# Kernel tuning notes

Hardware: AMD Instinct MI355X
Metric: run time of the kernel (lower is better)

## Reference

```python
import jax, jax.numpy as jnp
import numpy as np
from jax import lax

LN_EPS = 1e-5

D_MODEL, N_HEADS, HEAD_DIM, RANK, POWER_K = 1024, 16, 64, 32, 4
RIDGE_EPS, SPECTRAL_GAMMA = 1e-4, 0.99


def setup_inputs() -> dict:
    key = jax.random.key(0)
    ks = jax.random.split(key, 8)
    B, T = 4, 4096
    s = 1.0 / np.sqrt(D_MODEL)
    inp = {
        "hidden_states": jax.random.normal(ks[0], (B, T, D_MODEL), dtype=jnp.float32),
        "Wk": jax.random.normal(ks[1], (D_MODEL, N_HEADS * RANK), dtype=jnp.float32) * s,
        "Wq": jax.random.normal(ks[2], (D_MODEL, N_HEADS * RANK), dtype=jnp.float32) * s,
        "Wv": jax.random.normal(ks[3], (D_MODEL, N_HEADS * HEAD_DIM), dtype=jnp.float32) * s,
        "Wo": jax.random.normal(ks[4], (N_HEADS * HEAD_DIM, D_MODEL), dtype=jnp.float32) * s,
        "ln_scale": jnp.ones((D_MODEL,), jnp.float32),
        "ln_bias": jnp.zeros((D_MODEL,), jnp.float32),
        "gate_alpha": jnp.zeros((1,), jnp.float32),
        "log_ridge": jnp.array(np.log(RIDGE_EPS), jnp.float32),
        "log_gamma": jnp.array(np.log(SPECTRAL_GAMMA), jnp.float32),
        "prefix_len": 2048,
    }
    return inp


def _tri_solve(L, b, transpose=False):
    # solves L x = b (or L^T x = b) with lower-triangular L; batched over leading dims
    return lax.linalg.triangular_solve(L, b, left_side=True, lower=True, transpose_a=transpose)


def _build_operator(keys, values, ridge, gamma):
    # keys: (B,H,L,r), values: (B,H,L,dh)
    r = keys.shape[-1]
    G = jnp.einsum('bhlr,bhls->bhrs', keys, keys) + ridge * jnp.eye(r, dtype=keys.dtype)
    M = jnp.einsum('bhlr,bhls->bhrs', keys[:, :, 1:, :], keys[:, :, :-1, :])
    L = jnp.linalg.cholesky(G)                       # (B,H,r,r)
    U = _tri_solve(L, M)                             # L^{-1} M
    V = _tri_solve(L, jnp.swapaxes(U, -1, -2))       # L^{-1} (L^{-1}M)^T
    A_w = jnp.swapaxes(V, -1, -2)                    # L^{-1} M L^{-T}
    gamma_c = jnp.minimum(gamma, 1.0)
    sigma = jnp.linalg.svd(A_w, compute_uv=False)[..., 0]  # spectral norm
    sigma = jnp.maximum(sigma, 1e-8)
    scale = gamma_c / jnp.maximum(sigma, 1.0)
    A_w = A_w * scale[..., None, None]
    C_v = jnp.einsum('bhld,bhlr->bhdr', values, keys)       # (B,H,dh,r)
    Y = _tri_solve(L, jnp.swapaxes(C_v, -1, -2))            # L^{-1} C_v^T
    Bv_T = _tri_solve(L, Y, transpose=True)                 # G^{-1} C_v^T
    B_v = jnp.swapaxes(Bv_T, -1, -2)                        # (B,H,dh,r)
    return A_w, L, B_v


def _spectral_filter(A_w, L, B_v, queries, power_K):
    # queries: (B,H,Q,r) -> (B,H,Q,dh)
    qT = jnp.swapaxes(queries, -1, -2)      # (B,H,r,Q)
    w = _tri_solve(L, qT)                   # whiten
    for _ in range(power_K):
        w = jnp.matmul(A_w, w)
    z_hat = jnp.matmul(L, w)                # unwhiten
    out = jnp.matmul(B_v, z_hat)            # (B,H,dh,Q)
    return jnp.swapaxes(out, -1, -2)


def reference(hidden_states, Wk, Wq, Wv, Wo, ln_scale, ln_bias,
              gate_alpha, log_ridge, log_gamma, prefix_len):
    B, T, D = hidden_states.shape
    P = max(1, min(int(prefix_len), T - 1))
    mu = jnp.mean(hidden_states, axis=-1, keepdims=True)
    var = jnp.var(hidden_states, axis=-1, keepdims=True)
    normed = (hidden_states - mu) / jnp.sqrt(var + LN_EPS) * ln_scale + ln_bias
    def proj(W, dim):
        y = normed @ W
        return jnp.swapaxes(y.reshape(B, T, N_HEADS, dim), 1, 2)  # (B,H,T,dim)
    keys_all = proj(Wk, RANK)
    queries_all = proj(Wq, RANK)
    values_all = proj(Wv, HEAD_DIM)
    ridge = jnp.exp(log_ridge)
    gamma = jnp.exp(log_gamma)
    A_w, L, B_v = _build_operator(keys_all[:, :, :P, :], values_all[:, :, :P, :], ridge, gamma)
    q_out = _spectral_filter(A_w, L, B_v, queries_all[:, :, P:, :], POWER_K)
    p_out = _spectral_filter(A_w, L, B_v, keys_all[:, :, :P, :], POWER_K)
    full = jnp.concatenate([p_out, q_out], axis=2)               # (B,H,T,dh)
    full = jnp.swapaxes(full, 1, 2).reshape(B, T, N_HEADS * HEAD_DIM)
    out = full @ Wo
    return jax.nn.sigmoid(gate_alpha) * out
```

## Files before the change

kernel.cpp:

```cpp
#include <hip/hip_runtime.h>
#include <math.h>

#define D_MODEL 1024
#define TT 4096
#define NB 4
#define NH 16
#define TCH 8

typedef __attribute__((ext_vector_type(8))) short s8v;
typedef __attribute__((ext_vector_type(4))) float f4v;
typedef __attribute__((ext_vector_type(8))) unsigned short u16x8;

#define OFF_STATS ((size_t)0)
#define OFF_GP    ((size_t)(1) << 20)
#define OFF_MP    ((size_t)(3) << 20)
#define OFF_CP    ((size_t)(5) << 20)
#define OFF_FT    ((size_t)(9) << 20)
#define OFF_WKH   ((size_t)(10) << 20)
#define OFF_WKL   ((size_t)(11) << 20)
#define OFF_WQH   ((size_t)(12) << 20)
#define OFF_WQL   ((size_t)(13) << 20)
#define OFF_WVH   ((size_t)(14) << 20)
#define OFF_WVL   ((size_t)(16) << 20)
#define OFF_WOH   ((size_t)(18) << 20)
#define OFF_WOL   ((size_t)(20) << 20)
#define OFF_Y1    ((size_t)(22) << 20)
#define OFF_Y2    ((size_t)(54) << 20)
#define OFF_FH    OFF_Y2

__device__ __forceinline__ unsigned short bf16_rne(float x) {
  unsigned u = __float_as_uint(x);
  return (unsigned short)((u + 0x7fffu + ((u >> 16) & 1u)) >> 16);
}
__device__ __forceinline__ void split_bf16(float x, unsigned short& h, unsigned short& l) {
  unsigned u = __float_as_uint(x);
  unsigned r = (u + 0x7fffu + ((u >> 16) & 1u)) & 0xffff0000u;
  h = (unsigned short)(r >> 16);
  float res = x - __uint_as_float(r);
  l = bf16_rne(res);
}

__device__ __forceinline__ void gll16(unsigned short* lds, const unsigned short* g) {
  __builtin_amdgcn_global_load_lds(
      (__attribute__((address_space(1))) void*)(void*)(g),
      (__attribute__((address_space(3))) void*)(lds), 16, 0, 0);
}

__device__ __forceinline__ void xcd_swz(int gx, int gy, int& x, int& y, int& z) {
  int wg = blockIdx.x + gx * (blockIdx.y + gy * blockIdx.z);
  int k = wg & 7, j = wg >> 3;
  x = j % gx;
  int yz = k + ((j / gx) << 3);
  y = yz % gy;
  z = yz / gy;
}

__global__ __launch_bounds__(256) void ln_stats_k(const float* __restrict__ X,
                                                  float* __restrict__ stats) {
  int r = blockIdx.x;
  const float4 v = ((const float4*)(X + (size_t)r * D_MODEL))[threadIdx.x];
  float s  = v.x + v.y + v.z + v.w;
  float ss = v.x * v.x + v.y * v.y + v.z * v.z + v.w * v.w;
#pragma unroll
  for (int off = 32; off > 0; off >>= 1) {
    s  += __shfl_down(s, off, 64);
    ss += __shfl_down(ss, off, 64);
  }
  __shared__ float as_[4], bs_[4];
  int w = threadIdx.x >> 6, lane = threadIdx.x & 63;
  if (lane == 0) { as_[w] = s; bs_[w] = ss; }
  __syncthreads();
  if (threadIdx.x == 0) {
    float S  = as_[0] + as_[1] + as_[2] + as_[3];
    float SS = bs_[0] + bs_[1] + bs_[2] + bs_[3];
    float mu  = S * (1.0f / D_MODEL);
    float var = SS * (1.0f / D_MODEL) - mu * mu;
    stats[2 * (size_t)r]     = mu;
    stats[2 * (size_t)r + 1] = 1.0f / sqrtf(var + 1e-5f);
  }
}

__global__ __launch_bounds__(256) void prep_w_k(const float* __restrict__ W, int N,
                                                unsigned short* __restrict__ Thi,
                                                unsigned short* __restrict__ Tlo) {
  __shared__ float tileT[32 * 33];
  const int n0 = blockIdx.x * 32, k0 = blockIdx.y * 32;
  const int tid = threadIdx.x;
  {
    int k_l = tid >> 3, n4 = (tid & 7) << 2;
    float4 v = *(const float4*)&W[(size_t)(k0 + k_l) * N + n0 + n4];
    tileT[(n4 + 0) * 33 + k_l] = v.x;
    tileT[(n4 + 1) * 33 + k_l] = v.y;
    tileT[(n4 + 2) * 33 + k_l] = v.z;
    tileT[(n4 + 3) * 33 + k_l] = v.w;
  }
  __syncthreads();
  {
    int n_l = tid >> 3, k4 = (tid & 7) << 2;
    unsigned short h[4], l[4];
#pragma unroll
    for (int i = 0; i < 4; i++) split_bf16(tileT[n_l * 33 + k4 + i], h[i], l[i]);
    *(ushort4*)&Thi[(size_t)(n0 + n_l) * 1024 + k0 + k4] = make_ushort4(h[0], h[1], h[2], h[3]);
    *(ushort4*)&Tlo[(size_t)(n0 + n_l) * 1024 + k0 + k4] = make_ushort4(l[0], l[1], l[2], l[3]);
  }
}

__global__ __launch_bounds__(256) void gemm_proj_k(
    const float* __restrict__ X, const float* __restrict__ stats,
    const float* __restrict__ lng, const float* __restrict__ lnb,
    const unsigned short* __restrict__ WThi, const unsigned short* __restrict__ WTlo,
    int Nw, const int* __restrict__ pref, int mode, float* __restrict__ Y) {
  int P = pref[0]; P = P < 1 ? 1 : (P > TT - 1 ? TT - 1 : P);
  int xx, yy, zz;
  xcd_swz(8, 32, xx, yy, zz);
  const int b  = zz;
  const int t0 = yy * 128;
  const int n0 = xx * 128;
  if (mode == 1) { if (t0 + 128 <= P) return; }
  else           { if (t0 >= P) return; }
  const int row0 = b * TT + t0;
  __shared__ __align__(16) unsigned short Ah[128 * 40], Al[128 * 40];
  __shared__ __align__(16) unsigned short Bh[128 * 32], Bl[128 * 32];
  __shared__ float mus[128], rss[128];
  const int tid = threadIdx.x;
  if (tid < 128) {
    mus[tid] = stats[2 * (size_t)(row0 + tid)];
    rss[tid] = stats[2 * (size_t)(row0 + tid) + 1];
  }
  const int lane = tid & 63;
  const int wid  = tid >> 6;
  const int wm = (wid >> 1) * 64, wn = (wid & 1) * 64;
  const int lm = lane & 15, lq = lane >> 4;
  const int srow = lane >> 2, scol = (lane & 3) << 3;
  f4v acc[4][4];
#pragma unroll
  for (int i = 0; i < 4; i++)
#pragma unroll
    for (int j = 0; j < 4; j++) acc[i][j] = (f4v){0.f, 0.f, 0.f, 0.f};

  for (int kt = 0; kt < D_MODEL; kt += 32) {
    __syncthreads();
#pragma unroll
    for (int s = 0; s < 2; s++) {
      int seg = wid * 2 + s;
      int brow = n0 + seg * 16 + srow;
      gll16(&Bh[seg * 512], &WThi[(size_t)brow * 1024 + kt + scol]);
      gll16(&Bl[seg * 512], &WTlo[(size_t)brow * 1024 + kt + scol]);
    }
#pragma unroll
    for (int q = 0; q < 2; q++) {
      int c = tid * 2 + q;
      int m = c >> 2, k8 = (c & 3) << 3;
      const float* src = &X[(size_t)(row0 + m) * D_MODEL + kt + k8];
      float mu = mus[m], rs = rss[m];
      u16x8 hv, lv;
#pragma unroll
      for (int i = 0; i < 8; i++) {
        float nv = (src[i] - mu) * rs * lng[kt + k8 + i] + lnb[kt + k8 + i];
        unsigned short h, l;
        split_bf16(nv, h, l);
        hv[i] = h; lv[i] = l;
      }
      *(u16x8*)&Ah[m * 40 + k8] = hv;
      *(u16x8*)&Al[m * 40 + k8] = lv;
    }
    __syncthreads();
    s8v ah[4], al[4], bh[4], bl[4];
#pragma unroll
    for (int i = 0; i < 4; i++) {
      int ar = (wm + i * 16 + lm) * 40 + lq * 8;
      int br = (wn + i * 16 + lm) * 32 + lq * 8;
      ah[i] = *(const s8v*)&Ah[ar];
      al[i] = *(const s8v*)&Al[ar];
      bh[i] = *(const s8v*)&Bh[br];
      bl[i] = *(const s8v*)&Bl[br];
    }
#pragma unroll
    for (int mi = 0; mi < 4; mi++)
#pragma unroll
      for (int ni = 0; ni < 4; ni++) {
        acc[mi][ni] = __builtin_amdgcn_mfma_f32_16x16x32_bf16(ah[mi], bh[ni], acc[mi][ni], 0, 0, 0);
        acc[mi][ni] = __builtin_amdgcn_mfma_f32_16x16x32_bf16(ah[mi], bl[ni], acc[mi][ni], 0, 0, 0);
        acc[mi][ni] = __builtin_amdgcn_mfma_f32_16x16x32_bf16(al[mi], bh[ni], acc[mi][ni], 0, 0, 0);
      }
  }
#pragma unroll
  for (int mi = 0; mi < 4; mi++) {
#pragma unroll
    for (int r = 0; r < 4; r++) {
      int t = t0 + wm + mi * 16 + lq * 4 + r;
      bool ok = (mode == 1) ? (t >= P) : (t < P);
      if (!ok) continue;
      size_t orow = (mode == 2) ? ((size_t)b * P + t) : ((size_t)b * TT + t);
#pragma unroll
      for (int ni = 0; ni < 4; ni++)
        Y[orow * Nw + n0 + wn + ni * 16 + lm] = acc[mi][ni][r];
    }
  }
}

__global__ __launch_bounds__(256) void gemm_kq_k(
    const float* __restrict__ X, const float* __restrict__ stats,
    const float* __restrict__ lng, const float* __restrict__ lnb,
    const unsigned short* __restrict__ KH, const unsigned short* __restrict__ KL,
    const unsigned short* __restrict__ QH, const unsigned short* __restrict__ QL,
    const int* __restrict__ pref, float* __restrict__ Y) {
  int P = pref[0]; P = P < 1 ? 1 : (P > TT - 1 ? TT - 1 : P);
  int xx, yy, zz;
  xcd_swz(4, 32, xx, yy, zz);
  const int b  = zz;
  const int t0 = yy * 128;
  const int n0 = xx * 128;
  const int row0 = b * TT + t0;
  const bool hasK = (t0 < P);
  const bool hasQ = (t0 + 128 > P);
  __shared__ __align__(16) unsigned short Ah[128 * 40], Al[128 * 40];
  __shared__ __align__(16) unsigned short Bh[128 * 32], Bl[128 * 32];
  __shared__ float mus[128], rss[128];
  const int tid = threadIdx.x;
  if (tid < 128) {
    mus[tid] = stats[2 * (size_t)(row0 + tid)];
    rss[tid] = stats[2 * (size_t)(row0 + tid) + 1];
  }
  const int lane = tid & 63;
  const int wid  = tid >> 6;
  const int wm = (wid >> 1) * 64, wn = (wid & 1) * 64;
  const int lm = lane & 15, lq = lane >> 4;
  const int srow = lane >> 2, scol = (lane & 3) << 3;

  for (int pass = 0; pass < 2; pass++) {
    if (pass == 0 && !hasK) continue;
    if (pass == 1 && !hasQ) continue;
    const unsigned short* WThi = pass ? QH : KH;
    const unsigned short* WTlo = pass ? QL : KL;
    f4v acc[4][4];
#pragma unroll
    for (int i = 0; i < 4; i++)
#pragma unroll
      for (int j = 0; j < 4; j++) acc[i][j] = (f4v){0.f, 0.f, 0.f, 0.f};

    for (int kt = 0; kt < D_MODEL; kt += 32) {
      __syncthreads();
#pragma unroll
      for (int s = 0; s < 2; s++) {
        int seg = wid * 2 + s;
        int brow = n0 + seg * 16 + srow;
        gll16(&Bh[seg * 512], &WThi[(size_t)brow * 1024 + kt + scol]);
        gll16(&Bl[seg * 512], &WTlo[(size_t)brow * 1024 + kt + scol]);
      }
#pragma unroll
      for (int q = 0; q < 2; q++) {
        int c = tid * 2 + q;
        int m = c >> 2, k8 = (c & 3) << 3;
        const float* src = &X[(size_t)(row0 + m) * D_MODEL + kt + k8];
        float mu = mus[m], rs = rss[m];
        u16x8 hv, lv;
#pragma unroll
        for (int i = 0; i < 8; i++) {
          float nv = (src[i] - mu) * rs * lng[kt + k8 + i] + lnb[kt + k8 + i];
          unsigned short h, l;
          split_bf16(nv, h, l);
          hv[i] = h; lv[i] = l;
        }
        *(u16x8*)&Ah[m * 40 + k8] = hv;
        *(u16x8*)&Al[m * 40 + k8] = lv;
      }
      __syncthreads();
      s8v ah[4], al[4], bh[4], bl[4];
#pragma unroll
      for (int i = 0; i < 4; i++) {
        int ar = (wm + i * 16 + lm) * 40 + lq * 8;
        int br = (wn + i * 16 + lm) * 32 + lq * 8;
        ah[i] = *(const s8v*)&Ah[ar];
        al[i] = *(const s8v*)&Al[ar];
        bh[i] = *(const s8v*)&Bh[br];
        bl[i] = *(const s8v*)&Bl[br];
      }
#pragma unroll
      for (int mi = 0; mi < 4; mi++)
#pragma unroll
        for (int ni = 0; ni < 4; ni++) {
          acc[mi][ni] = __builtin_amdgcn_mfma_f32_16x16x32_bf16(ah[mi], bh[ni], acc[mi][ni], 0, 0, 0);
          acc[mi][ni] = __builtin_amdgcn_mfma_f32_16x16x32_bf16(ah[mi], bl[ni], acc[mi][ni], 0, 0, 0);
          acc[mi][ni] = __builtin_amdgcn_mfma_f32_16x16x32_bf16(al[mi], bh[ni], acc[mi][ni], 0, 0, 0);
        }
    }
#pragma unroll
    for (int mi = 0; mi < 4; mi++) {
#pragma unroll
      for (int r = 0; r < 4; r++) {
        int t = t0 + wm + mi * 16 + lq * 4 + r;
        bool ok = pass ? (t >= P) : (t < P);
        if (!ok) continue;
#pragma unroll
        for (int ni = 0; ni < 4; ni++)
          Y[((size_t)b * TT + t) * 512 + n0 + wn + ni * 16 + lm] = acc[mi][ni][r];
      }
    }
  }
}

__global__ __launch_bounds__(256) void build_gmc_mfma_k(
    const float* __restrict__ Y1, const float* __restrict__ Y2,
    const int* __restrict__ pref,
    float* __restrict__ Gp, float* __restrict__ Mp, float* __restrict__ Cp) {
  int P = pref[0]; P = P < 1 ? 1 : (P > TT - 1 ? TT - 1 : P);
  const int c  = blockIdx.x;
  const int bh = blockIdx.y;
  const int b = bh >> 4, h = bh & 15;
  const int chunk = (P + TCH - 1) / TCH;
  const int tb = c * chunk;
  const int te = min(tb + chunk, P);

  __shared__ __align__(16) unsigned short kCh[32 * 136], kCl[32 * 136];
  __shared__ __align__(16) unsigned short kPh[32 * 136], kPl[32 * 136];
  __shared__ __align__(16) unsigned short vTh[64 * 136], vTl[64 * 136];

  const int tid = threadIdx.x;
  const int wid = tid >> 6, lane = tid & 63;
  const int lm = lane & 15, lq = lane >> 4;

  f4v acc[4];
#pragma unroll
  for (int i = 0; i < 4; i++) acc[i] = (f4v){0.f, 0.f, 0.f, 0.f};

  for (int t0 = tb; t0 < te; t0 += 128) {
    const int len = (te - t0 < 128) ? (te - t0) : 128;
    __syncthreads();
    for (int e = tid; e < 129 * 8; e += 256) {
      int row = e >> 3, j4 = (e & 7) << 2;
      int t = t0 - 1 + row;
      float4 kv = make_float4(0.f, 0.f, 0.f, 0.f);
      if (row <= len && t >= 0)
        kv = *(const float4*)&Y1[((size_t)b * TT + t) * 512 + h * 32 + j4];
      unsigned short hh[4], ll[4];
      split_bf16(kv.x, hh[0], ll[0]); split_bf16(kv.y, hh[1], ll[1]);
      split_bf16(kv.z, hh[2], ll[2]); split_bf16(kv.w, hh[3], ll[3]);
      if (row >= 1) {
#pragma unroll
        for (int q = 0; q < 4; q++) {
          kCh[(j4 + q) * 136 + row - 1] = hh[q];
          kCl[(j4 + q) * 136 + row - 1] = ll[q];
        }
      }
      if (row < 128) {
#pragma unroll
        for (int q = 0; q < 4; q++) {
          kPh[(j4 + q) * 136 + row] = hh[q];
          kPl[(j4 + q) * 136 + row] = ll[q];
        }
      }
    }
    for (int e = tid; e < 128 * 16; e += 256) {
      int row = e >> 4, dj = (e & 15) << 2;
      int t = t0 + row;
      float4 vv = make_float4(0.f, 0.f, 0.f, 0.f);
      if (row < len)
        vv = *(const float4*)&Y2[((size_t)b * P + t) * 1024 + h * 64 + dj];
      unsigned short hh[4], ll[4];
      split_bf16(vv.x, hh[0], ll[0]); split_bf16(vv.y, hh[1], ll[1]);
      split_bf16(vv.z, hh[2], ll[2]); split_bf16(vv.w, hh[3], ll[3]);
#pragma unroll
      for (int q = 0; q < 4; q++) {
        vTh[(dj + q) * 136 + row] = hh[q];
        vTl[(dj + q) * 136 + row] = ll[q];
      }
    }
    __syncthreads();

#pragma unroll
    for (int kk = 0; kk < 128; kk += 32) {
      const int off = kk + lq * 8;
      if (wid == 0) {
        s8v h0 = *(const s8v*)&kCh[(0 + lm) * 136 + off];
        s8v h1 = *(const s8v*)&kCh[(16 + lm) * 136 + off];
        s8v l0 = *(const s8v*)&kCl[(0 + lm) * 136 + off];
        s8v l1 = *(const s8v*)&kCl[(16 + lm) * 136 + off];
        acc[0] = __builtin_amdgcn_mfma_f32_16x16x32_bf16(h0, h0, acc[0], 0, 0, 0);
        acc[0] = __builtin_amdgcn_mfma_f32_16x16x32_bf16(h0, l0, acc[0], 0, 0, 0);
        acc[0] = __builtin_amdgcn_mfma_f32_16x16x32_bf16(l0, h0, acc[0], 0, 0, 0);
        acc[1] = __builtin_amdgcn_mfma_f32_16x16x32_bf16(h0, h1, acc[1], 0, 0, 0);
        acc[1] = __builtin_amdgcn_mfma_f32_16x16x32_bf16(h0, l1, acc[1], 0, 0, 0);
        acc[1] = __builtin_amdgcn_mfma_f32_16x16x32_bf16(l0, h1, acc[1], 0, 0, 0);
        acc[2] = __builtin_amdgcn_mfma_f32_16x16x32_bf16(h1, h0, acc[2], 0, 0, 0);
        acc[2] = __builtin_amdgcn_mfma_f32_16x16x32_bf16(h1, l0, acc[2], 0, 0, 0);
        acc[2] = __builtin_amdgcn_mfma_f32_16x16x32_bf16(l1, h0, acc[2], 0, 0, 0);
        acc[3] = __builtin_amdgcn_mfma_f32_16x16x32_bf16(h1, h1, acc[3], 0, 0, 0);
        acc[3] = __builtin_amdgcn_mfma_f32_16x16x32_bf16(h1, l1, acc[3], 0, 0, 0);
        acc[3] = __builtin_amdgcn_mfma_f32_16x16x32_bf16(l1, h1, acc[3], 0, 0, 0);
      } else if (wid == 1) {
        s8v ah0 = *(const s8v*)&kCh[(0 + lm) * 136 + off];
        s8v ah1 = *(const s8v*)&kCh[(16 + lm) * 136 + off];
        s8v al0 = *(const s8v*)&kCl[(0 + lm) * 136 + off];
        s8v al1 = *(const s8v*)&kCl[(16 + lm) * 136 + off];
        s8v bh0 = *(const s8v*)&kPh[(0 + lm) * 136 + off];
        s8v bh1 = *(const s8v*)&kPh[(16 + lm) * 136 + off];
        s8v bl0 = *(const s8v*)&kPl[(0 + lm) * 136 + off];
        s8v bl1 = *(const s8v*)&kPl[(16 + lm) * 136 + off];
        acc[0] = __builtin_amdgcn_mfma_f32_16x16x32_bf16(ah0, bh0, acc[0], 0, 0, 0);
        acc[0] = __builtin_amdgcn_mfma_f32_16x16x32_bf16(ah0, bl0, acc[0], 0, 0, 0);
        acc[0] = __builtin_amdgcn_mfma_f32_16x16x32_bf16(al0, bh0, acc[0], 0, 0, 0);
        acc[1] = __builtin_amdgcn_mfma_f32_16x16x32_bf16(ah0, bh1, acc[1], 0, 0, 0);
        acc[1] = __builtin_amdgcn_mfma_f32_16x16x32_bf16(ah0, bl1, acc[1], 0, 0, 0);
        acc[1] = __builtin_amdgcn_mfma_f32_16x16x32_bf16(al0, bh1, acc[1], 0, 0, 0);
        acc[2] = __builtin_amdgcn_mfma_f32_16x16x32_bf16(ah1, bh0, acc[2], 0, 0, 0);
        acc[2] = __builtin_amdgcn_mfma_f32_16x16x32_bf16(ah1, bl0, acc[2], 0, 0, 0);
        acc[2] = __builtin_amdgcn_mfma_f32_16x16x32_bf16(al1, bh0, acc[2], 0, 0, 0);
        acc[3] = __builtin_amdgcn_mfma_f32_16x16x32_bf16(ah1, bh1, acc[3], 0, 0, 0);
        acc[3] = __builtin_amdgcn_mfma_f32_16x16x32_bf16(ah1, bl1, acc[3], 0, 0, 0);
        acc[3] = __builtin_amdgcn_mfma_f32_16x16x32_bf16(al1, bh1, acc[3], 0, 0, 0);
      } else {
        const int d0 = (wid - 2) * 32;
        s8v vh0 = *(const s8v*)&vTh[(d0 + lm) * 136 + off];
        s8v vh1 = *(const s8v*)&vTh[(d0 + 16 + lm) * 136 + off];
        s8v vl0 = *(const s8v*)&vTl[(d0 + lm) * 136 + off];
        s8v vl1 = *(const s8v*)&vTl[(d0 + 16 + lm) * 136 + off];
        s8v kh0 = *(const s8v*)&kCh[(0 + lm) * 136 + off];
        s8v kh1 = *(const s8v*)&kCh[(16 + lm) * 136 + off];
        s8v kl0 = *(const s8v*)&kCl[(0 + lm) * 136 + off];
        s8v kl1 = *(const s8v*)&kCl[(16 + lm) * 136 + off];
        acc[0] = __builtin_amdgcn_mfma_f32_16x16x32_bf16(vh0, kh0, acc[0], 0, 0, 0);
        acc[0] = __builtin_amdgcn_mfma_f32_16x16x32_bf16(vh0, kl0, acc[0], 0, 0, 0);
        acc[0] = __builtin_amdgcn_mfma_f32_16x16x32_bf16(vl0, kh0, acc[0], 0, 0, 0);
        acc[1] = __builtin_amdgcn_mfma_f32_16x16x32_bf16(vh0, kh1, acc[1], 0, 0, 0);
        acc[1] = __builtin_amdgcn_mfma_f32_16x16x32_bf16(vh0, kl1, acc[1], 0, 0, 0);
        acc[1] = __builtin_amdgcn_mfma_f32_16x16x32_bf16(vl0, kh1, acc[1], 0, 0, 0);
        acc[2] = __builtin_amdgcn_mfma_f32_16x16x32_bf16(vh1, kh0, acc[2], 0, 0, 0);
        acc[2] = __builtin_amdgcn_mfma_f32_16x16x32_bf16(vh1, kl0, acc[2], 0, 0, 0);
        acc[2] = __builtin_amdgcn_mfma_f32_16x16x32_bf16(vl1, kh0, acc[2], 0, 0, 0);
        acc[3] = __builtin_amdgcn_mfma_f32_16x16x32_bf16(vh1, kh1, acc[3], 0, 0, 0);
        acc[3] = __builtin_amdgcn_mfma_f32_16x16x32_bf16(vh1, kl1, acc[3], 0, 0, 0);
        acc[3] = __builtin_amdgcn_mfma_f32_16x16x32_bf16(vl1, kh1, acc[3], 0, 0, 0);
      }
    }
  }

  if (wid < 2) {
    float* dst = (wid == 0 ? Gp : Mp) + (size_t)(c * 64 + bh) * 1024;
#pragma unroll
    for (int t = 0; t < 4; t++) {
      int i0 = (t >> 1) * 16, j0 = (t & 1) * 16;
#pragma unroll
      for (int r = 0; r < 4; r++)
        dst[(i0 + lq * 4 + r) * 32 + j0 + lm] = acc[t][r];
    }
  } else {
    float* dst = Cp + (size_t)(c * 64 + bh) * 2048;
#pragma unroll
    for (int t = 0; t < 4; t++) {
      int d0 = (wid - 2) * 32 + (t >> 1) * 16, j0 = (t & 1) * 16;
#pragma unroll
      for (int r = 0; r < 4; r++)
        dst[(d0 + lq * 4 + r) * 32 + j0 + lm] = acc[t][r];
    }
  }
}

__global__ __launch_bounds__(256) void solve_op_k(
    const float* __restrict__ Gp, const float* __restrict__ Mp,
    const float* __restrict__ Cp, const float* __restrict__ lridge,
    const float* __restrict__ lgamma, float* __restrict__ Ft) {
  __shared__ float Gs[32 * 33];
  __shared__ float Ms[32 * 32];
  __shared__ float Gi[32 * 32];
  __shared__ float W1[32 * 33];
  __shared__ float Aw[32 * 33];
  __shared__ float Nn[32 * 32];
  __shared__ float N2[32 * 32];
  __shared__ float T1[32 * 32];
  __shared__ float Cs[64 * 32];
  __shared__ float red[256];
  __shared__ float vv[32], uu[32];
  const int bh = blockIdx.x;
  const int tid = threadIdx.x;
  const float ridge = expf(lridge[0]);

  for (int e = tid; e < 1024; e += 256) {
    int i = e >> 5, j = e & 31;
    float g = 0.f, m = 0.f;
#pragma unroll
    for (int cc = 0; cc < TCH; cc++) {
      g += Gp[(size_t)(cc * 64 + bh) * 1024 + e];
      m += Mp[(size_t)(cc * 64 + bh) * 1024 + e];
    }
    if (i == j) g += ridge;
    Gs[i * 33 + j] = g;
    Ms[e] = m;
  }
  for (int e = tid; e < 2048; e += 256) {
    float s = 0.f;
#pragma unroll
    for (int cc = 0; cc < TCH; cc++) s += Cp[(size_t)(cc * 64 + bh) * 2048 + e];
    Cs[e] = s;
  }
  __syncthreads();

  for (int j = 0; j < 32; j++) {
    float d = Gs[j * 33 + j];
    __syncthreads();
    float inv = 1.0f / sqrtf(d);
    if (tid >= j && tid < 32) Gs[tid * 33 + j] *= inv;
    __syncthreads();
    int w = 31 - j;
    for (int e = tid; e < w * w; e += 256) {
      int i = j + 1 + e / w, k = j + 1 + e % w;
      Gs[i * 33 + k] -= Gs[i * 33 + j] * Gs[k * 33 + j];
    }
    __syncthreads();
  }

  if (tid < 32) {
    const int c = tid;
    for (int i = 0; i < 32; i++) W1[i * 33 + c] = (i == c) ? 1.0f : 0.0f;
    for (int i = 0; i < 32; i++) {
      float s = W1[i * 33 + c];
      for (int j = 0; j < i; j++) s -= Gs[i * 33 + j] * W1[j * 33 + c];
      W1[i * 33 + c] = s / Gs[i * 33 + i];
    }
    for (int i = 31; i >= 0; i--) {
      float s = W1[i * 33 + c];
      for (int j = i + 1; j < 32; j++) s -= Gs[j * 33 + i] * W1[j * 33 + c];
      W1[i * 33 + c] = s / Gs[i * 33 + i];
    }
    for (int i = 0; i < 32; i++) Gi[i * 32 + c] = W1[i * 33 + c];
  }
  __syncthreads();
  if (tid < 32) {
    const int c = tid;
    for (int i = 0; i < 32; i++) {
      float s = Ms[i * 32 + c];
      for (int j = 0; j < i; j++) s -= Gs[i * 33 + j] * W1[j * 33 + c];
      W1[i * 33 + c] = s / Gs[i * 33 + i];
    }
  }
  __syncthreads();
  if (tid < 32) {
    const int c = tid;
    for (int i = 0; i < 32; i++) {
      float s = W1[c * 33 + i];
      for (int j = 0; j < i; j++) s -= Gs[i * 33 + j] * Aw[j * 33 + c];
      Aw[i * 33 + c] = s / Gs[i * 33 + i];
    }
  }
  __syncthreads();

  float s0 = 0.0f;
  for (int e = tid; e < 1024; e += 256) {
    float a = Aw[(e >> 5) * 33 + (e & 31)];
    s0 += a * a;
  }
  red[tid] = s0;
  __syncthreads();
  for (int off = 128; off > 0; off >>= 1) {
    if (tid < off) red[tid] += red[tid + off];
    __syncthreads();
  }
  float frob2 = red[0];
  float sigma;
  if (frob2 <= 1.0f) {
    sigma = sqrtf(frob2);
  } else {
    if (tid < 32) vv[tid] = 1.0f + 0.001f * (float)tid;
    __syncthreads();
    for (int it = 0; it < 64; it++) {
      if (tid < 32) {
        float s = 0;
        for (int j = 0; j < 32; j++) s += Aw[tid * 33 + j] * vv[j];
        uu[tid] = s;
      }
      __syncthreads();
      if (tid == 0) {
        float n = 0;
        for (int j = 0; j < 32; j++) n += uu[j] * uu[j];
        red[0] = sqrtf(n);
      }
      __syncthreads();
      float nu = fmaxf(red[0], 1e-30f);
      if (tid < 32) uu[tid] /= nu;
      __syncthreads();
      if (tid < 32) {
        float s = 0;
        for (int j = 0; j < 32; j++) s += Aw[j * 33 + tid] * uu[j];
        vv[tid] = s;
      }
      __syncthreads();
      if (tid == 0) {
        float n = 0;
        for (int j = 0; j < 32; j++) n += vv[j] * vv[j];
        red[0] = sqrtf(n);
      }
      __syncthreads();
      float nv = fmaxf(red[0], 1e-30f);
      if (tid < 32) vv[tid] /= nv;
      __syncthreads();
    }
    sigma = red[0];
  }
  float gamma_c = fminf(expf(lgamma[0]), 1.0f);
  float scale = gamma_c / fmaxf(fmaxf(sigma, 1e-8f), 1.0f);

  for (int e = tid; e < 1024; e += 256) {
    int i = e >> 5, c = e & 31;
    float s = 0;
#pragma unroll
    for (int k = 0; k < 32; k++) s += Ms[i * 32 + k] * Gi[k * 32 + c];
    Nn[e] = scale * s;
  }
  __syncthreads();
  for (int e = tid; e < 1024; e += 256) {
    int i = e >> 5, c = e & 31;
    float s = 0;
#pragma unroll
    for (int k = 0; k < 32; k++) s += Nn[i * 32 + k] * Nn[k * 32 + c];
    N2[e] = s;
  }
  __syncthreads();
  for (int e = tid; e < 1024; e += 256) {
    int i = e >> 5, c = e & 31;
    float s = 0;
#pragma unroll
    for (int k = 0; k < 32; k++) s += N2[i * 32 + k] * N2[k * 32 + c];
    Ms[e] = s;
  }
  __syncthreads();
  for (int e = tid; e < 1024; e += 256) {
    int i = e >> 5, c = e & 31;
    float s = 0;
#pragma unroll
    for (int k = 0; k < 32; k++) s += Gi[i * 32 + k] * Ms[k * 32 + c];
    T1[e] = s;
  }
  __syncthreads();
  for (int e = tid; e < 2048; e += 256) {
    int j = e >> 6, d = e & 63;
    float s = 0;
#pragma unroll
    for (int k = 0; k < 32; k++) s += Cs[d * 32 + k] * T1[k * 32 + j];
    Ft[(size_t)bh * 2048 + e] = s;
  }
}

__global__ __launch_bounds__(256) void apply_k(const float* __restrict__ Y1,
                                               const float* __restrict__ Ft,
                                               unsigned short* __restrict__ FH) {
  __shared__ float xs[128 * 32];
  const int h = blockIdx.y;
  const int r0 = blockIdx.x * 128;
  const int bh = (r0 >> 12) * NH + h;
  const int tid = threadIdx.x;
  const int d = tid & 63, t0 = tid >> 6;
  float fcol[32];
  const float* fb = &Ft[(size_t)bh * 2048 + d];
#pragma unroll
  for (int j = 0; j < 32; j++) fcol[j] = fb[j * 64];
  for (int e = tid; e < 1024; e += 256) {
    int row = e >> 3, j4 = (e & 7) << 2;
    *(float4*)&xs[row * 32 + j4] =
        *(const float4*)&Y1[((size_t)(r0 + row)) * 512 + h * 32 + j4];
  }
  __syncthreads();
  for (int tl = t0; tl < 128; tl += 4) {
    float s = 0;
#pragma unroll
    for (int j = 0; j < 32; j++) s += xs[tl * 32 + j] * fcol[j];
    FH[((size_t)(r0 + tl)) * 1024 + h * 64 + d] = bf16_rne(s);
  }
}

__global__ __launch_bounds__(256) void gemm_out_k(
    const unsigned short* __restrict__ FH,
    const unsigned short* __restrict__ WThi, const unsigned short* __restrict__ WTlo,
    const float* __restrict__ alpha, float* __restrict__ out) {
  int xx, yy, zz;
  xcd_swz(8, 128, xx, yy, zz);
  const int m0 = yy * 128;
  const int n0 = xx * 128;
  __shared__ __align__(16) unsigned short Ah[128 * 32];
  __shared__ __align__(16) unsigned short Bh[128 * 32], Bl[128 * 32];
  const int tid = threadIdx.x;
  const int lane = tid & 63;
  const int wid  = tid >> 6;
  const int wm = (wid >> 1) * 64, wn = (wid & 1) * 64;
  const int lm = lane & 15, lq = lane >> 4;
  const int srow = lane >> 2, scol = (lane & 3) << 3;
  f4v acc[4][4];
#pragma unroll
  for (int i = 0; i < 4; i++)
#pragma unroll
    for (int j = 0; j < 4; j++) acc[i][j] = (f4v){0.f, 0.f, 0.f, 0.f};

  for (int kt = 0; kt < D_MODEL; kt += 32) {
    __syncthreads();
#pragma unroll
    for (int s = 0; s < 2; s++) {
      int seg = wid * 2 + s;
      int row = seg * 16 + srow;
      gll16(&Ah[seg * 512], &FH  [(size_t)(m0 + row) * 1024 + kt + scol]);
      gll16(&Bh[seg * 512], &WThi[(size_t)(n0 + row) * 1024 + kt + scol]);
      gll16(&Bl[seg * 512], &WTlo[(size_t)(n0 + row) * 1024 + kt + scol]);
    }
    __syncthreads();
    s8v ah[4], bh[4], bl[4];
#pragma unroll
    for (int i = 0; i < 4; i++) {
      ah[i] = *(const s8v*)&Ah[(wm + i * 16 + lm) * 32 + lq * 8];
      bh[i] = *(const s8v*)&Bh[(wn + i * 16 + lm) * 32 + lq * 8];
      bl[i] = *(const s8v*)&Bl[(wn + i * 16 + lm) * 32 + lq * 8];
    }
#pragma unroll
    for (int mi = 0; mi < 4; mi++)
#pragma unroll
      for (int ni = 0; ni < 4; ni++) {
        acc[mi][ni] = __builtin_amdgcn_mfma_f32_16x16x32_bf16(ah[mi], bh[ni], acc[mi][ni], 0, 0, 0);
        acc[mi][ni] = __builtin_amdgcn_mfma_f32_16x16x32_bf16(ah[mi], bl[ni], acc[mi][ni], 0, 0, 0);
      }
  }
  float sg = 1.0f / (1.0f + expf(-alpha[0]));
#pragma unroll
  for (int mi = 0; mi < 4; mi++)
#pragma unroll
    for (int r = 0; r < 4; r++) {
      size_t orow = (size_t)(m0 + wm + mi * 16 + lq * 4 + r);
#pragma unroll
      for (int ni = 0; ni < 4; ni++)
        out[orow * 1024 + n0 + wn + ni * 16 + lm] = sg * acc[mi][ni][r];
    }
}

extern "C" void kernel_launch(void* const* d_in, const int* in_sizes, int n_in,
                              void* d_out, int out_size, void* d_ws, size_t ws_size,
                              hipStream_t stream) {
  const float* X      = (const float*)d_in[0];
  const float* Wk     = (const float*)d_in[1];
  const float* Wq     = (const float*)d_in[2];
  const float* Wv     = (const float*)d_in[3];
  const float* Wo     = (const float*)d_in[4];
  const float* lng    = (const float*)d_in[5];
  const float* lnb    = (const float*)d_in[6];
  const float* alpha  = (const float*)d_in[7];
  const float* lridge = (const float*)d_in[8];
  const float* lgamma = (const float*)d_in[9];
  const int*   pref   = (const int*)d_in[10];
  float* out = (float*)d_out;
  char* ws = (char*)d_ws;
  float* stats = (float*)(ws + OFF_STATS);
  float* Gp    = (float*)(ws + OFF_GP);
  float* Mp    = (float*)(ws + OFF_MP);
  float* Cp    = (float*)(ws + OFF_CP);
  float* Ft    = (float*)(ws + OFF_FT);
  unsigned short* WKH = (unsigned short*)(ws + OFF_WKH);
  unsigned short* WKL = (unsigned short*)(ws + OFF_WKL);
  unsigned short* WQH = (unsigned short*)(ws + OFF_WQH);
  unsigned short* WQL = (unsigned short*)(ws + OFF_WQL);
  unsigned short* WVH = (unsigned short*)(ws + OFF_WVH);
  unsigned short* WVL = (unsigned short*)(ws + OFF_WVL);
  unsigned short* WOH = (unsigned short*)(ws + OFF_WOH);
  unsigned short* WOL = (unsigned short*)(ws + OFF_WOL);
  float* Y1 = (float*)(ws + OFF_Y1);
  float* Y2 = (float*)(ws + OFF_Y2);
  unsigned short* FH = (unsigned short*)(ws + OFF_FH);

  ln_stats_k<<<16384, 256, 0, stream>>>(X, stats);
  prep_w_k<<<dim3(16, 32), 256, 0, stream>>>(Wk, 512, WKH, WKL);
  prep_w_k<<<dim3(16, 32), 256, 0, stream>>>(Wq, 512, WQH, WQL);
  prep_w_k<<<dim3(32, 32), 256, 0, stream>>>(Wv, 1024, WVH, WVL);
  prep_w_k<<<dim3(32, 32), 256, 0, stream>>>(Wo, 1024, WOH, WOL);
  gemm_kq_k<<<dim3(4, 32, NB), 256, 0, stream>>>(X, stats, lng, lnb, WKH, WKL, WQH, WQL, pref, Y1);
  gemm_proj_k<<<dim3(8, 32, NB), 256, 0, stream>>>(X, stats, lng, lnb, WVH, WVL, 1024, pref, 2, Y2);
  build_gmc_mfma_k<<<dim3(TCH, 64), 256, 0, stream>>>(Y1, Y2, pref, Gp, Mp, Cp);
  solve_op_k<<<64, 256, 0, stream>>>(Gp, Mp, Cp, lridge, lgamma, Ft);
  apply_k<<<dim3(128, NH), 256, 0, stream>>>(Y1, Ft, FH);
  gemm_out_k<<<dim3(8, 128), 256, 0, stream>>>(FH, WOH, WOL, alpha, out);
}
```

Before: 467.4 us.

## Double-buffer output GEMM with XOR-swizzled operands and larger 256x128 tiles

```diff
diff --git a/kernel.cpp b/kernel.cpp
--- a/kernel.cpp
+++ b/kernel.cpp
@@ -82,7 +82,8 @@
 
 __global__ __launch_bounds__(256) void prep_w_k(const float* __restrict__ W, int N,
                                                 unsigned short* __restrict__ Thi,
-                                                unsigned short* __restrict__ Tlo) {
+                                                unsigned short* __restrict__ Tlo,
+                                                int swz) {
   __shared__ float tileT[32 * 33];
   const int n0 = blockIdx.x * 32, k0 = blockIdx.y * 32;
   const int tid = threadIdx.x;
@@ -100,8 +101,10 @@
     unsigned short h[4], l[4];
 #pragma unroll
     for (int i = 0; i < 4; i++) split_bf16(tileT[n_l * 33 + k4 + i], h[i], l[i]);
-    *(ushort4*)&Thi[(size_t)(n0 + n_l) * 1024 + k0 + k4] = make_ushort4(h[0], h[1], h[2], h[3]);
-    *(ushort4*)&Tlo[(size_t)(n0 + n_l) * 1024 + k0 + k4] = make_ushort4(l[0], l[1], l[2], l[3]);
+    int kc = k0 + k4;
+    int col = swz ? ((kc & ~63) | ((((kc >> 3) & 7) ^ (n_l & 7)) << 3) | (kc & 7)) : kc;
+    *(ushort4*)&Thi[(size_t)(n0 + n_l) * 1024 + col] = make_ushort4(h[0], h[1], h[2], h[3]);
+    *(ushort4*)&Tlo[(size_t)(n0 + n_l) * 1024 + col] = make_ushort4(l[0], l[1], l[2], l[3]);
   }
 }
 
@@ -659,62 +662,100 @@
         *(const float4*)&Y1[((size_t)(r0 + row)) * 512 + h * 32 + j4];
   }
   __syncthreads();
+  const int dq = d >> 3, dr = d & 7;
   for (int tl = t0; tl < 128; tl += 4) {
     float s = 0;
 #pragma unroll
     for (int j = 0; j < 32; j++) s += xs[tl * 32 + j] * fcol[j];
-    FH[((size_t)(r0 + tl)) * 1024 + h * 64 + d] = bf16_rne(s);
-  }
-}
-
-__global__ __launch_bounds__(256) void gemm_out_k(
+    int col = h * 64 + ((dq ^ (tl & 7)) << 3) + dr;
+    FH[((size_t)(r0 + tl)) * 1024 + col] = bf16_rne(s);
+  }
+}
+
+__global__ __launch_bounds__(512) void gemm_out_k(
     const unsigned short* __restrict__ FH,
     const unsigned short* __restrict__ WThi, const unsigned short* __restrict__ WTlo,
     const float* __restrict__ alpha, float* __restrict__ out) {
+  __shared__ __align__(16) unsigned short lds[65536];
   int xx, yy, zz;
-  xcd_swz(8, 128, xx, yy, zz);
-  const int m0 = yy * 128;
+  xcd_swz(8, 64, xx, yy, zz);
+  const int m0 = yy * 256;
   const int n0 = xx * 128;
-  __shared__ __align__(16) unsigned short Ah[128 * 32];
-  __shared__ __align__(16) unsigned short Bh[128 * 32], Bl[128 * 32];
   const int tid = threadIdx.x;
   const int lane = tid & 63;
   const int wid  = tid >> 6;
-  const int wm = (wid >> 1) * 64, wn = (wid & 1) * 64;
+  const int wm = (wid >> 1) * 64;
+  const int wn = (wid & 1) * 64;
   const int lm = lane & 15, lq = lane >> 4;
-  const int srow = lane >> 2, scol = (lane & 3) << 3;
+  const int l8 = lane >> 3, c8 = (lane & 7) << 3;
+
   f4v acc[4][4];
 #pragma unroll
   for (int i = 0; i < 4; i++)
 #pragma unroll
     for (int j = 0; j < 4; j++) acc[i][j] = (f4v){0.f, 0.f, 0.f, 0.f};
 
-  for (int kt = 0; kt < D_MODEL; kt += 32) {
-    __syncthreads();
-#pragma unroll
-    for (int s = 0; s < 2; s++) {
-      int seg = wid * 2 + s;
-      int row = seg * 16 + srow;
-      gll16(&Ah[seg * 512], &FH  [(size_t)(m0 + row) * 1024 + kt + scol]);
-      gll16(&Bh[seg * 512], &WThi[(size_t)(n0 + row) * 1024 + kt + scol]);
-      gll16(&Bl[seg * 512], &WTlo[(size_t)(n0 + row) * 1024 + kt + scol]);
-    }
-    __syncthreads();
-    s8v ah[4], bh[4], bl[4];
+  auto STAGE = [&](int t, int buf) {
+    const int kt = t * 64;
 #pragma unroll
     for (int i = 0; i < 4; i++) {
-      ah[i] = *(const s8v*)&Ah[(wm + i * 16 + lm) * 32 + lq * 8];
-      bh[i] = *(const s8v*)&Bh[(wn + i * 16 + lm) * 32 + lq * 8];
-      bl[i] = *(const s8v*)&Bl[(wn + i * 16 + lm) * 32 + lq * 8];
-    }
-#pragma unroll
-    for (int mi = 0; mi < 4; mi++)
-#pragma unroll
-      for (int ni = 0; ni < 4; ni++) {
-        acc[mi][ni] = __builtin_amdgcn_mfma_f32_16x16x32_bf16(ah[mi], bh[ni], acc[mi][ni], 0, 0, 0);
-        acc[mi][ni] = __builtin_amdgcn_mfma_f32_16x16x32_bf16(ah[mi], bl[ni], acc[mi][ni], 0, 0, 0);
-      }
-  }
+      int iss = wid * 4 + i;
+      gll16(&lds[buf * 16384 + iss * 512],
+            &FH[(size_t)(m0 + iss * 8 + l8) * 1024 + kt + c8]);
+    }
+#pragma unroll
+    for (int i = 0; i < 2; i++) {
+      int iss = wid * 2 + i;
+      gll16(&lds[32768 + buf * 8192 + iss * 512],
+            &WThi[(size_t)(n0 + iss * 8 + l8) * 1024 + kt + c8]);
+    }
+#pragma unroll
+    for (int i = 0; i < 2; i++) {
+      int iss = wid * 2 + i;
+      gll16(&lds[49152 + buf * 8192 + iss * 512],
+            &WTlo[(size_t)(n0 + iss * 8 + l8) * 1024 + kt + c8]);
+    }
+  };
+
+  STAGE(0, 0);
+  STAGE(1, 1);
+
+  for (int t = 0; t < 16; t++) {
+    const int buf = t & 1;
+    if (t < 15) asm volatile("s_waitcnt vmcnt(8)" ::: "memory");
+    else        asm volatile("s_waitcnt vmcnt(0)" ::: "memory");
+    __builtin_amdgcn_s_barrier();
+    const unsigned short* Ab  = &lds[buf * 16384];
+    const unsigned short* Bhb = &lds[32768 + buf * 8192];
+    const unsigned short* Blb = &lds[49152 + buf * 8192];
+    __builtin_amdgcn_s_setprio(1);
+#pragma unroll
+    for (int kk = 0; kk < 2; kk++) {
+      s8v ah[4], bh[4], bl[4];
+#pragma unroll
+      for (int i = 0; i < 4; i++) {
+        int rA = wm + i * 16 + lm;
+        int rB = wn + i * 16 + lm;
+        int sA = (((kk * 4 + lq) ^ (rA & 7)) << 3);
+        int sB = (((kk * 4 + lq) ^ (rB & 7)) << 3);
+        ah[i] = *(const s8v*)&Ab[rA * 64 + sA];
+        bh[i] = *(const s8v*)&Bhb[rB * 64 + sB];
+        bl[i] = *(const s8v*)&Blb[rB * 64 + sB];
+      }
+#pragma unroll
+      for (int mi = 0; mi < 4; mi++)
+#pragma unroll
+        for (int ni = 0; ni < 4; ni++) {
+          acc[mi][ni] = __builtin_amdgcn_mfma_f32_16x16x32_bf16(ah[mi], bh[ni], acc[mi][ni], 0, 0, 0);
+          acc[mi][ni] = __builtin_amdgcn_mfma_f32_16x16x32_bf16(ah[mi], bl[ni], acc[mi][ni], 0, 0, 0);
+        }
+    }
+    __builtin_amdgcn_s_setprio(0);
+    __builtin_amdgcn_sched_barrier(0);
+    __builtin_amdgcn_s_barrier();
+    if (t < 14) STAGE(t + 2, buf);
+  }
+
   float sg = 1.0f / (1.0f + expf(-alpha[0]));
 #pragma unroll
   for (int mi = 0; mi < 4; mi++)
@@ -761,14 +802,14 @@
   unsigned short* FH = (unsigned short*)(ws + OFF_FH);
 
   ln_stats_k<<<16384, 256, 0, stream>>>(X, stats);
-  prep_w_k<<<dim3(16, 32), 256, 0, stream>>>(Wk, 512, WKH, WKL);
-  prep_w_k<<<dim3(16, 32), 256, 0, stream>>>(Wq, 512, WQH, WQL);
-  prep_w_k<<<dim3(32, 32), 256, 0, stream>>>(Wv, 1024, WVH, WVL);
-  prep_w_k<<<dim3(32, 32), 256, 0, stream>>>(Wo, 1024, WOH, WOL);
+  prep_w_k<<<dim3(16, 32), 256, 0, stream>>>(Wk, 512, WKH, WKL, 0);
+  prep_w_k<<<dim3(16, 32), 256, 0, stream>>>(Wq, 512, WQH, WQL, 0);
+  prep_w_k<<<dim3(32, 32), 256, 0, stream>>>(Wv, 1024, WVH, WVL, 0);
+  prep_w_k<<<dim3(32, 32), 256, 0, stream>>>(Wo, 1024, WOH, WOL, 1);
   gemm_kq_k<<<dim3(4, 32, NB), 256, 0, stream>>>(X, stats, lng, lnb, WKH, WKL, WQH, WQL, pref, Y1);
   gemm_proj_k<<<dim3(8, 32, NB), 256, 0, stream>>>(X, stats, lng, lnb, WVH, WVL, 1024, pref, 2, Y2);
   build_gmc_mfma_k<<<dim3(TCH, 64), 256, 0, stream>>>(Y1, Y2, pref, Gp, Mp, Cp);
   solve_op_k<<<64, 256, 0, stream>>>(Gp, Mp, Cp, lridge, lgamma, Ft);
   apply_k<<<dim3(128, NH), 256, 0, stream>>>(Y1, Ft, FH);
-  gemm_out_k<<<dim3(8, 128), 256, 0, stream>>>(FH, WOH, WOL, alpha, out);
-}
+  gemm_out_k<<<dim3(8, 64), 512, 0, stream>>>(FH, WOH, WOL, alpha, out);
+}
```

Result: no change. 461.8 us (-1.2%).
